# Kernel optimization log

Measured on AMD Instinct MI355X. Metric: run time of the kernel, lower is better.

Reference implementation:

```python
import jax, jax.numpy as jnp
import numpy as np

B, N, CIN, K = 4, 4096, 64, 16
MLP = [64, 64, 128]
EPS = 1e-5


def setup_inputs() -> dict:
    key = jax.random.key(0)
    ks = jax.random.split(key, 8)
    inp = {
        "xyz": jax.random.normal(ks[0], (B, N, 3), dtype=jnp.float32),
        "points": jax.random.normal(ks[1], (B, N, CIN), dtype=jnp.float32),
    }
    last = 3 + CIN
    for i, oc in enumerate(MLP):
        inp[f"w{i}"] = jax.random.normal(ks[2 + i], (oc, last), dtype=jnp.float32) * 0.05
        inp[f"b{i}"] = jnp.zeros((oc,), dtype=jnp.float32)
        inp[f"g{i}"] = jnp.ones((oc,), dtype=jnp.float32)
        inp[f"be{i}"] = jnp.zeros((oc,), dtype=jnp.float32)
        inp[f"rm{i}"] = jnp.zeros((oc,), dtype=jnp.float32)
        inp[f"rv{i}"] = jnp.ones((oc,), dtype=jnp.float32)
        last = oc
    return inp


def reference(xyz, points, w0, b0, g0, be0, rm0, rv0,
              w1, b1, g1, be1, rm1, rv1,
              w2, b2, g2, be2, rm2, rv2):
    # knn via squared pairwise distance (same argsort order as cdist)
    sq = jnp.sum(xyz * xyz, axis=-1)  # (B,N)
    d2 = sq[:, :, None] + sq[:, None, :] - 2.0 * jnp.einsum('bnc,bmc->bnm', xyz, xyz)
    _, idx = jax.lax.top_k(-d2, K)  # (B,N,K), smallest-distance neighbors

    bidx = jnp.arange(xyz.shape[0])[:, None, None]  # (B,1,1)
    grouped_xyz = xyz[bidx, idx] - xyz[:, :, None, :]     # (B,N,K,3) relative coords
    grouped_pts = points[bidx, idx]                        # (B,N,K,CIN)
    h = jnp.concatenate([grouped_xyz, grouped_pts], axis=-1)  # (B,N,K,3+CIN)

    layers = [(w0, b0, g0, be0, rm0, rv0),
              (w1, b1, g1, be1, rm1, rv1),
              (w2, b2, g2, be2, rm2, rv2)]
    for (w, b, g, be, rm, rv) in layers:
        # 1x1 conv == per-point linear; BN in eval mode (running stats)
        h = jnp.einsum('bnkc,oc->bnko', h, w) + b
        h = (h - rm) * jax.lax.rsqrt(rv + EPS) * g + be
        h = jax.nn.relu(h)
    new_points = jnp.max(h, axis=2)  # max over K neighbors -> (B,N,C_out)
    return new_points
```

## Files before the change

kernel.cpp:

```cpp
#include <hip/hip_runtime.h>

#define NPT   4096
#define KNN_K 16
#define EPSV  1e-5f

#define W1T_OFF 4352
#define B1_OFF  8448
#define W2T_OFF 8512
#define B2_OFF  16704
#define IDX_OFF 16832
#define P_OFF   344512
#define Q_OFF   1393088

typedef unsigned long long ull;

__device__ __forceinline__ ull minu64(ull a, ull b) { return a < b ? a : b; }
__device__ __forceinline__ ull maxu64(ull a, ull b) { return a > b ? a : b; }

__device__ __forceinline__ ull bitonic_sort64(ull v, int lane) {
#pragma unroll
  for (int k = 2; k <= 64; k <<= 1) {
#pragma unroll
    for (int j = k >> 1; j > 0; j >>= 1) {
      ull o = __shfl_xor(v, j);
      bool lower = (lane & j) == 0;
      bool up = (lane & k) == 0;
      v = (lower == up) ? minu64(v, o) : maxu64(v, o);
    }
  }
  return v;
}

__device__ __forceinline__ ull bitonic_merge64(ull v, int lane) {
#pragma unroll
  for (int j = 32; j > 0; j >>= 1) {
    ull o = __shfl_xor(v, j);
    v = ((lane & j) == 0) ? minu64(v, o) : maxu64(v, o);
  }
  return v;
}

__device__ __forceinline__ void filter_step(float4 q, float4 c, unsigned idx32,
                                            unsigned& thresh_hi, int& cnt,
                                            ull& R, ull* buf, int lane) {
  float dot = __fadd_rn(__fadd_rn(__fmul_rn(q.x, c.x), __fmul_rn(q.y, c.y)),
                        __fmul_rn(q.z, c.z));
  float d2 = __fsub_rn(__fadd_rn(q.w, c.w), __fmul_rn(2.0f, dot));
  unsigned bits = __float_as_uint(d2);
  unsigned fk = bits ^ (0x80000000u | (unsigned)((int)bits >> 31));
  bool pred = fk <= thresh_hi;
  ull mask = __ballot(pred);
  if (mask) {
    int pos = cnt + (int)__builtin_amdgcn_mbcnt_hi(
                        (unsigned)(mask >> 32),
                        __builtin_amdgcn_mbcnt_lo((unsigned)mask, 0u));
    if (pred) buf[pos] = ((ull)fk << 32) | idx32;
    cnt += __popcll(mask);
    if (cnt >= 64) {
      ull v = buf[lane];
      v = bitonic_sort64(v, lane);
      ull vr = __shfl(v, 63 - lane);
      R = minu64(R, vr);
      R = bitonic_merge64(R, lane);
      thresh_hi = (unsigned)__shfl((int)(unsigned)(R >> 32), 15);
      cnt -= 64;
      if (lane < cnt) {
        ull tmp = buf[64 + lane];
        buf[lane] = tmp;
      }
    }
  }
}

__device__ __forceinline__ ull final_flush(ull R, int cnt, ull* buf, int lane) {
  ull v = (lane < cnt) ? buf[lane] : ~0ull;
  v = bitonic_sort64(v, lane);
  ull vr = __shfl(v, 63 - lane);
  R = minu64(R, vr);
  return bitonic_merge64(R, lane);
}

__global__ __launch_bounds__(256) void mega_kernel(
    const float* __restrict__ xyz, const float* __restrict__ points,
    const float* __restrict__ w0, const float* __restrict__ b0, const float* __restrict__ g0,
    const float* __restrict__ be0, const float* __restrict__ rm0, const float* __restrict__ rv0,
    const float* __restrict__ w1, const float* __restrict__ b1, const float* __restrict__ g1,
    const float* __restrict__ be1, const float* __restrict__ rm1, const float* __restrict__ rv1,
    const float* __restrict__ w2, const float* __restrict__ b2, const float* __restrict__ g2,
    const float* __restrict__ be2, const float* __restrict__ rm2, const float* __restrict__ rv2,
    float* __restrict__ ws, int* __restrict__ knnOut) {
  __shared__ __align__(16) unsigned char smem[20480];
  int blk = blockIdx.x;
  int tid = threadIdx.x;

  if (blk < 2048) {
    ull* bufb = (ull*)smem;
    int lane = tid & 63, w = tid >> 6;
    int b = blk >> 9;
    int n0 = ((blk & 511) << 3) + (w << 1);
    int n1 = n0 + 1;
    const float* xb = xyz + (size_t)b * NPT * 3;
    ull* buf0 = bufb + w * 256;
    ull* buf1 = buf0 + 128;

    float4 q0, q1;
    {
      const float* qp = xb + n0 * 3;
      float ax = qp[0], ay = qp[1], az = qp[2];
      float bx = qp[3], by = qp[4], bz = qp[5];
      q0 = make_float4(ax, ay, az,
          __fadd_rn(__fadd_rn(__fmul_rn(ax, ax), __fmul_rn(ay, ay)), __fmul_rn(az, az)));
      q1 = make_float4(bx, by, bz,
          __fadd_rn(__fadd_rn(__fmul_rn(bx, bx), __fmul_rn(by, by)), __fmul_rn(bz, bz)));
    }
    ull R0 = ~0ull, R1 = ~0ull;
    unsigned th0 = 0xFFFFFFFFu, th1 = 0xFFFFFFFFu;
    int cnt0 = 0, cnt1 = 0;

    float cx = xb[3 * lane], cy = xb[3 * lane + 1], cz = xb[3 * lane + 2];
#pragma unroll 1
    for (int g = 0; g < NPT; g += 64) {
      int ni = 3 * ((g + 64 + lane) & (NPT - 1));
      float nx = xb[ni], ny = xb[ni + 1], nz = xb[ni + 2];
      float csq = __fadd_rn(__fadd_rn(__fmul_rn(cx, cx), __fmul_rn(cy, cy)),
                            __fmul_rn(cz, cz));
      float4 c = make_float4(cx, cy, cz, csq);
      unsigned idx32 = (unsigned)(g + lane);
      filter_step(q0, c, idx32, th0, cnt0, R0, buf0, lane);
      filter_step(q1, c, idx32, th1, cnt1, R1, buf1, lane);
      cx = nx; cy = ny; cz = nz;
    }
    R0 = final_flush(R0, cnt0, buf0, lane);
    R1 = final_flush(R1, cnt1, buf1, lane);
    if (lane < KNN_K) {
      knnOut[(b * NPT + n0) * KNN_K + lane] = (int)(unsigned)(R0 & 0xFFFFFFFFull);
      knnOut[(b * NPT + n1) * KNN_K + lane] = (int)(unsigned)(R1 & 0xFFFFFFFFull);
    }
    return;
  }

  if (blk < 4096) {
    float* wlds = (float*)smem;
    for (int j = tid; j < 4288; j += 256) {
      int r = j / 67;
      float s = g0[r] * rsqrtf(rv0[r] + EPSV);
      wlds[j] = __fmul_rn(w0[j], s);
    }
    __syncthreads();
    int oc = tid & 63;
    int base = (blk - 2048) * 8 + (tid >> 6);
    float s = g0[oc] * rsqrtf(rv0[oc] + EPSV);
    float b0f = (b0[oc] - rm0[oc]) * s + be0[oc];
    const float* wrow = wlds + oc * 67;
#pragma unroll 1
    for (int pt = 0; pt < 2; ++pt) {
      int i = base + pt * 4;
      float x = xyz[i * 3], y = xyz[i * 3 + 1], z = xyz[i * 3 + 2];
      float qacc = wrow[0] * x;
      qacc = fmaf(wrow[1], y, qacc);
      qacc = fmaf(wrow[2], z, qacc);
      float acc = b0f + qacc;
      const float* prow = points + (size_t)i * 64;
#pragma unroll 4
      for (int c = 0; c < 64; ++c) acc = fmaf(wrow[3 + c], prow[c], acc);
      ws[P_OFF + (size_t)i * 64 + oc] = acc;
      ws[Q_OFF + (size_t)i * 64 + oc] = qacc;
    }
    return;
  }

  {
    int i = (blk - 4096) * 256 + tid + 4352;
    if (i < 8448) {
      int j = i - 4352; int oc = j & 63, ic = j >> 6;
      float s = g1[oc] * rsqrtf(rv1[oc] + EPSV);
      ws[i] = w1[oc * 64 + ic] * s;
    } else if (i < 8512) {
      int oc = i - 8448;
      float s = g1[oc] * rsqrtf(rv1[oc] + EPSV);
      ws[i] = (b1[oc] - rm1[oc]) * s + be1[oc];
    } else if (i < 16704) {
      int j = i - 8512; int ic = j >> 7, oc = j & 127;
      float s = g2[oc] * rsqrtf(rv2[oc] + EPSV);
      ws[i] = w2[oc * 64 + ic] * s;
    } else if (i < 16832) {
      int oc = i - 16704;
      float s = g2[oc] * rsqrtf(rv2[oc] + EPSV);
      ws[i] = (b2[oc] - rm2[oc]) * s + be2[oc];
    }
  }
}

__global__ __launch_bounds__(256, 3) void mlp_kernel(
    const float* __restrict__ wbuf, const int* __restrict__ knn,
    float* __restrict__ out) {
  __shared__ __align__(16) float Ash[64 * 128];
  __shared__ __align__(16) float Wsh[32 * 128];
  int tid = threadIdx.x;
  int qblk = blockIdx.x << 3;

  const float4* w1g = (const float4*)(wbuf + W1T_OFF);
  const float4* w2g = (const float4*)(wbuf + W2T_OFF);
  float4* wl = (float4*)Wsh;

#define W2C(e, h) ((((h) << 5) + ((e) >> 5)) * 32 + ((e) & 31))

  float4 s0 = w1g[tid];
  float4 s1 = w1g[256 + tid];
  float4 s2, s3;

  {
    int p = tid & 127, half = tid >> 7;
    int q = qblk + (p >> 4);
    int k = p & 15;
    int src = knn[q * KNN_K + k];
    int srow = (q & ~(NPT - 1)) + src;
    const float4* Pp = (const float4*)(wbuf + P_OFF + (size_t)srow * 64 + half * 32);
    const float4* Qp = (const float4*)(wbuf + Q_OFF + (size_t)q * 64 + half * 32);
#pragma unroll
    for (int j = 0; j < 8; ++j) {
      float4 pv = Pp[j];
      float4 qv = Qp[j];
      int ic = half * 32 + j * 4;
      Ash[(ic + 0) * 128 + p] = fmaxf(pv.x - qv.x, 0.0f);
      Ash[(ic + 1) * 128 + p] = fmaxf(pv.y - qv.y, 0.0f);
      Ash[(ic + 2) * 128 + p] = fmaxf(pv.z - qv.z, 0.0f);
      Ash[(ic + 3) * 128 + p] = fmaxf(pv.w - qv.w, 0.0f);
    }
  }
  wl[tid] = s0; wl[256 + tid] = s1;
  s0 = w1g[512 + tid]; s1 = w1g[768 + tid];
  __syncthreads();

  int og = tid & 7, pg = tid >> 3;
  const float* Arow = Ash + 4 * pg;
  const float* Wrow = Wsh + 8 * og;
  float acc[8][8];

#define GEMM32(R0)                                                        \
  _Pragma("unroll 8")                                                     \
  for (int ic = 0; ic < 32; ++ic) {                                       \
    float4 a0 = *(const float4*)(Arow + ((R0) + ic) * 128);               \
    float4 wv0 = *(const float4*)(Wrow + ic * 64);                        \
    float4 wv1 = *(const float4*)(Wrow + ic * 64 + 4);                    \
    float av[4] = {a0.x, a0.y, a0.z, a0.w};                               \
    float wv[8] = {wv0.x, wv0.y, wv0.z, wv0.w, wv1.x, wv1.y, wv1.z, wv1.w};\
    _Pragma("unroll")                                                     \
    for (int ii = 0; ii < 4; ++ii)                                        \
      _Pragma("unroll")                                                   \
      for (int jj = 0; jj < 8; ++jj) acc[ii][jj] = fmaf(av[ii], wv[jj], acc[ii][jj]); \
  }

  {
    float4 b0v = *(const float4*)(wbuf + B1_OFF + 8 * og);
    float4 b1v = *(const float4*)(wbuf + B1_OFF + 8 * og + 4);
    float bj[8] = {b0v.x, b0v.y, b0v.z, b0v.w, b1v.x, b1v.y, b1v.z, b1v.w};
#pragma unroll
    for (int i = 0; i < 4; ++i)
#pragma unroll
      for (int j = 0; j < 8; ++j) acc[i][j] = bj[j];
  }
  GEMM32(0)
  __syncthreads();
  wl[tid] = s0; wl[256 + tid] = s1;
  s0 = w2g[W2C(tid, 0)];       s1 = w2g[W2C(tid + 256, 0)];
  s2 = w2g[W2C(tid + 512, 0)]; s3 = w2g[W2C(tid + 768, 0)];
  __syncthreads();
  GEMM32(32)
  __syncthreads();

#pragma unroll
  for (int j = 0; j < 8; ++j) {
    int oc = 8 * og + j;
    *(float4*)(Ash + oc * 128 + 4 * pg) =
        make_float4(fmaxf(acc[0][j], 0.0f), fmaxf(acc[1][j], 0.0f),
                    fmaxf(acc[2][j], 0.0f), fmaxf(acc[3][j], 0.0f));
  }
  wl[tid] = s0; wl[256 + tid] = s1; wl[512 + tid] = s2; wl[768 + tid] = s3;
  s0 = w2g[W2C(tid, 1)];       s1 = w2g[W2C(tid + 256, 1)];
  s2 = w2g[W2C(tid + 512, 1)]; s3 = w2g[W2C(tid + 768, 1)];
  __syncthreads();

  int og2 = tid & 15, pg2 = tid >> 4;
  const float* Arow2 = Ash + 8 * pg2;
  const float* Wrow2 = Wsh + 8 * og2;

#define GEMM32L2(R0)                                                      \
  _Pragma("unroll 4")                                                     \
  for (int ic = 0; ic < 32; ++ic) {                                       \
    float4 a0 = *(const float4*)(Arow2 + ((R0) + ic) * 128);              \
    float4 a1 = *(const float4*)(Arow2 + ((R0) + ic) * 128 + 4);          \
    float4 wv0 = *(const float4*)(Wrow2 + ic * 128);                      \
    float4 wv1 = *(const float4*)(Wrow2 + ic * 128 + 4);                  \
    float av[8] = {a0.x, a0.y, a0.z, a0.w, a1.x, a1.y, a1.z, a1.w};       \
    float wv[8] = {wv0.x, wv0.y, wv0.z, wv0.w, wv1.x, wv1.y, wv1.z, wv1.w};\
    _Pragma("unroll")                                                     \
    for (int ii = 0; ii < 8; ++ii)                                        \
      _Pragma("unroll")                                                   \
      for (int jj = 0; jj < 8; ++jj) acc[ii][jj] = fmaf(av[ii], wv[jj], acc[ii][jj]); \
  }

  {
    float4 b0v = *(const float4*)(wbuf + B2_OFF + 8 * og2);
    float4 b1v = *(const float4*)(wbuf + B2_OFF + 8 * og2 + 4);
    float bj[8] = {b0v.x, b0v.y, b0v.z, b0v.w, b1v.x, b1v.y, b1v.z, b1v.w};
#pragma unroll
    for (int i = 0; i < 8; ++i)
#pragma unroll
      for (int j = 0; j < 8; ++j) acc[i][j] = bj[j];
  }
  GEMM32L2(0)
  __syncthreads();
  wl[tid] = s0; wl[256 + tid] = s1; wl[512 + tid] = s2; wl[768 + tid] = s3;
  __syncthreads();
  GEMM32L2(32)

  {
    int qout = qblk + (pg2 >> 1);
    float* obase = out + (size_t)qout * 128 + 8 * og2;
    float m[8];
#pragma unroll
    for (int j = 0; j < 8; ++j) {
      float v = fmaxf(fmaxf(fmaxf(acc[0][j], acc[1][j]), fmaxf(acc[2][j], acc[3][j])),
                      fmaxf(fmaxf(acc[4][j], acc[5][j]), fmaxf(acc[6][j], acc[7][j])));
      v = fmaxf(v, 0.0f);
      m[j] = fmaxf(v, __shfl_xor(v, 16));
    }
    if ((pg2 & 1) == 0) {
      *(float4*)(obase)     = make_float4(m[0], m[1], m[2], m[3]);
      *(float4*)(obase + 4) = make_float4(m[4], m[5], m[6], m[7]);
    }
  }
#undef GEMM32
#undef GEMM32L2
#undef W2C
}

extern "C" void kernel_launch(void* const* d_in, const int* in_sizes, int n_in,
                              void* d_out, int out_size, void* d_ws, size_t ws_size,
                              hipStream_t stream) {
  const float* xyz    = (const float*)d_in[0];
  const float* points = (const float*)d_in[1];
  float* wsF = (float*)d_ws;
  int* idxBuf = (int*)(wsF + IDX_OFF);

  mega_kernel<<<4145, 256, 0, stream>>>(
      xyz, points,
      (const float*)d_in[2],  (const float*)d_in[3],  (const float*)d_in[4],
      (const float*)d_in[5],  (const float*)d_in[6],  (const float*)d_in[7],
      (const float*)d_in[8],  (const float*)d_in[9],  (const float*)d_in[10],
      (const float*)d_in[11], (const float*)d_in[12], (const float*)d_in[13],
      (const float*)d_in[14], (const float*)d_in[15], (const float*)d_in[16],
      (const float*)d_in[17], (const float*)d_in[18], (const float*)d_in[19],
      wsF, idxBuf);
  mlp_kernel<<<2048, 256, 0, stream>>>(wsF, idxBuf, (float*)d_out);
}
```

Measured before the change: 241.0 us.

## Split layer-2 GEMM into two 64-channel halves to cut registers and LDS

The final 64->128 layer is now computed as two 64-output-channel passes that reuse the layer-1 GEMM tiling (4x8 accumulators instead of 8x8). This halves the weight shared-memory tile and the accumulator registers, and the launch bound is raised from 3 to 4 blocks per SM. The max over the 16 neighbours now needs an extra cross-lane shuffle, and there are more barriers and weight staging steps in exchange for the higher occupancy.

```diff
diff --git a/kernel.cpp b/kernel.cpp
--- a/kernel.cpp
+++ b/kernel.cpp
@@ -191,11 +191,11 @@
   }
 }
 
-__global__ __launch_bounds__(256, 3) void mlp_kernel(
+__global__ __launch_bounds__(256, 4) void mlp_kernel(
     const float* __restrict__ wbuf, const int* __restrict__ knn,
     float* __restrict__ out) {
   __shared__ __align__(16) float Ash[64 * 128];
-  __shared__ __align__(16) float Wsh[32 * 128];
+  __shared__ __align__(16) float Wsh[32 * 64];
   int tid = threadIdx.x;
   int qblk = blockIdx.x << 3;
 
@@ -203,11 +203,10 @@
   const float4* w2g = (const float4*)(wbuf + W2T_OFF);
   float4* wl = (float4*)Wsh;
 
-#define W2C(e, h) ((((h) << 5) + ((e) >> 5)) * 32 + ((e) & 31))
+#define W2IDX(e, p, h) ((((h) << 5) + ((e) >> 4)) * 32 + ((p) << 4) + ((e) & 15))
 
   float4 s0 = w1g[tid];
   float4 s1 = w1g[256 + tid];
-  float4 s2, s3;
 
   {
     int p = tid & 127, half = tid >> 7;
@@ -235,7 +234,7 @@
   int og = tid & 7, pg = tid >> 3;
   const float* Arow = Ash + 4 * pg;
   const float* Wrow = Wsh + 8 * og;
-  float acc[8][8];
+  float acc[4][8];
 
 #define GEMM32(R0)                                                        \
   _Pragma("unroll 8")                                                     \
@@ -263,8 +262,7 @@
   GEMM32(0)
   __syncthreads();
   wl[tid] = s0; wl[256 + tid] = s1;
-  s0 = w2g[W2C(tid, 0)];       s1 = w2g[W2C(tid + 256, 0)];
-  s2 = w2g[W2C(tid + 512, 0)]; s3 = w2g[W2C(tid + 768, 0)];
+  s0 = w2g[W2IDX(tid, 0, 0)]; s1 = w2g[W2IDX(tid + 256, 0, 0)];
   __syncthreads();
   GEMM32(32)
   __syncthreads();
@@ -276,64 +274,77 @@
         make_float4(fmaxf(acc[0][j], 0.0f), fmaxf(acc[1][j], 0.0f),
                     fmaxf(acc[2][j], 0.0f), fmaxf(acc[3][j], 0.0f));
   }
-  wl[tid] = s0; wl[256 + tid] = s1; wl[512 + tid] = s2; wl[768 + tid] = s3;
-  s0 = w2g[W2C(tid, 1)];       s1 = w2g[W2C(tid + 256, 1)];
-  s2 = w2g[W2C(tid + 512, 1)]; s3 = w2g[W2C(tid + 768, 1)];
-  __syncthreads();
-
-  int og2 = tid & 15, pg2 = tid >> 4;
-  const float* Arow2 = Ash + 8 * pg2;
-  const float* Wrow2 = Wsh + 8 * og2;
-
-#define GEMM32L2(R0)                                                      \
-  _Pragma("unroll 4")                                                     \
-  for (int ic = 0; ic < 32; ++ic) {                                       \
-    float4 a0 = *(const float4*)(Arow2 + ((R0) + ic) * 128);              \
-    float4 a1 = *(const float4*)(Arow2 + ((R0) + ic) * 128 + 4);          \
-    float4 wv0 = *(const float4*)(Wrow2 + ic * 128);                      \
-    float4 wv1 = *(const float4*)(Wrow2 + ic * 128 + 4);                  \
-    float av[8] = {a0.x, a0.y, a0.z, a0.w, a1.x, a1.y, a1.z, a1.w};       \
-    float wv[8] = {wv0.x, wv0.y, wv0.z, wv0.w, wv1.x, wv1.y, wv1.z, wv1.w};\
-    _Pragma("unroll")                                                     \
-    for (int ii = 0; ii < 8; ++ii)                                        \
-      _Pragma("unroll")                                                   \
-      for (int jj = 0; jj < 8; ++jj) acc[ii][jj] = fmaf(av[ii], wv[jj], acc[ii][jj]); \
-  }
-
-  {
-    float4 b0v = *(const float4*)(wbuf + B2_OFF + 8 * og2);
-    float4 b1v = *(const float4*)(wbuf + B2_OFF + 8 * og2 + 4);
+  wl[tid] = s0; wl[256 + tid] = s1;
+  s0 = w2g[W2IDX(tid, 0, 1)]; s1 = w2g[W2IDX(tid + 256, 0, 1)];
+  __syncthreads();
+
+  int qout = qblk + (pg >> 2);
+  float* obase = out + (size_t)qout * 128 + 8 * og;
+
+  {
+    float4 b0v = *(const float4*)(wbuf + B2_OFF + 8 * og);
+    float4 b1v = *(const float4*)(wbuf + B2_OFF + 8 * og + 4);
     float bj[8] = {b0v.x, b0v.y, b0v.z, b0v.w, b1v.x, b1v.y, b1v.z, b1v.w};
 #pragma unroll
-    for (int i = 0; i < 8; ++i)
+    for (int i = 0; i < 4; ++i)
 #pragma unroll
       for (int j = 0; j < 8; ++j) acc[i][j] = bj[j];
   }
-  GEMM32L2(0)
-  __syncthreads();
-  wl[tid] = s0; wl[256 + tid] = s1; wl[512 + tid] = s2; wl[768 + tid] = s3;
-  __syncthreads();
-  GEMM32L2(32)
-
-  {
-    int qout = qblk + (pg2 >> 1);
-    float* obase = out + (size_t)qout * 128 + 8 * og2;
+  GEMM32(0)
+  __syncthreads();
+  wl[tid] = s0; wl[256 + tid] = s1;
+  s0 = w2g[W2IDX(tid, 1, 0)]; s1 = w2g[W2IDX(tid + 256, 1, 0)];
+  __syncthreads();
+  GEMM32(32)
+  {
     float m[8];
 #pragma unroll
     for (int j = 0; j < 8; ++j) {
-      float v = fmaxf(fmaxf(fmaxf(acc[0][j], acc[1][j]), fmaxf(acc[2][j], acc[3][j])),
-                      fmaxf(fmaxf(acc[4][j], acc[5][j]), fmaxf(acc[6][j], acc[7][j])));
+      float v = fmaxf(fmaxf(acc[0][j], acc[1][j]), fmaxf(acc[2][j], acc[3][j]));
       v = fmaxf(v, 0.0f);
+      v = fmaxf(v, __shfl_xor(v, 8));
       m[j] = fmaxf(v, __shfl_xor(v, 16));
     }
-    if ((pg2 & 1) == 0) {
+    if ((pg & 3) == 0) {
       *(float4*)(obase)     = make_float4(m[0], m[1], m[2], m[3]);
       *(float4*)(obase + 4) = make_float4(m[4], m[5], m[6], m[7]);
     }
   }
+  __syncthreads();
+  wl[tid] = s0; wl[256 + tid] = s1;
+  s0 = w2g[W2IDX(tid, 1, 1)]; s1 = w2g[W2IDX(tid + 256, 1, 1)];
+  __syncthreads();
+
+  {
+    float4 b0v = *(const float4*)(wbuf + B2_OFF + 64 + 8 * og);
+    float4 b1v = *(const float4*)(wbuf + B2_OFF + 64 + 8 * og + 4);
+    float bj[8] = {b0v.x, b0v.y, b0v.z, b0v.w, b1v.x, b1v.y, b1v.z, b1v.w};
+#pragma unroll
+    for (int i = 0; i < 4; ++i)
+#pragma unroll
+      for (int j = 0; j < 8; ++j) acc[i][j] = bj[j];
+  }
+  GEMM32(0)
+  __syncthreads();
+  wl[tid] = s0; wl[256 + tid] = s1;
+  __syncthreads();
+  GEMM32(32)
+  {
+    float m[8];
+#pragma unroll
+    for (int j = 0; j < 8; ++j) {
+      float v = fmaxf(fmaxf(acc[0][j], acc[1][j]), fmaxf(acc[2][j], acc[3][j]));
+      v = fmaxf(v, 0.0f);
+      v = fmaxf(v, __shfl_xor(v, 8));
+      m[j] = fmaxf(v, __shfl_xor(v, 16));
+    }
+    if ((pg & 3) == 0) {
+      *(float4*)(obase + 64)     = make_float4(m[0], m[1], m[2], m[3]);
+      *(float4*)(obase + 64 + 4) = make_float4(m[4], m[5], m[6], m[7]);
+    }
+  }
 #undef GEMM32
-#undef GEMM32L2
-#undef W2C
+#undef W2IDX
 }
 
 extern "C" void kernel_launch(void* const* d_in, const int* in_sizes, int n_in,
```

Measured after the change: 238.9 us. Within noise of the previous version (-0.9%).
